# Optimization experiments

Hardware: AMD Instinct MI355X
Metric: run time of the kernel (lower is better)

The kernel has to match this reference:

```python
import jax, jax.numpy as jnp
import numpy as np

D_MODEL = 1024
NUM_HEADS = 16
HEAD_DIM = D_MODEL // NUM_HEADS
THETA = 10000.0
B, S = 2, 2048


def _apply_rope(t, cos, sin):
    # t: [B, H, S, hd]; cos/sin: [S, hd//2]
    te = t[..., 0::2]
    to = t[..., 1::2]
    re = te * cos - to * sin
    ro = te * sin + to * cos
    out = jnp.stack([re, ro], axis=-1)  # [B,H,S,hd//2,2]
    return out.reshape(t.shape)


def setup_inputs() -> dict:
    key = jax.random.key(0)
    kx, kq, kk, kv, ko = jax.random.split(key, 5)
    std = 2.0 / (2 * D_MODEL) ** 0.5
    def w(k):
        return jnp.clip(std * jax.random.normal(k, (D_MODEL, D_MODEL), jnp.float32), -3.0 * std, 3.0 * std)
    return {
        "x": jax.random.normal(kx, (B, S, D_MODEL), jnp.float32),
        "Wq": w(kq),
        "Wk": w(kk),
        "Wv": w(kv),
        "Wo": w(ko),
    }


def reference(x, Wq, Wk, Wv, Wo):
    Bv, Sv, _ = x.shape
    def proj(W):
        return jnp.einsum('bsd,ed->bse', x, W).reshape(Bv, Sv, NUM_HEADS, HEAD_DIM).transpose(0, 2, 1, 3)
    q, k, v = proj(Wq), proj(Wk), proj(Wv)

    pos = jnp.arange(Sv, dtype=jnp.float32)
    inv_freq = THETA ** (-jnp.arange(0, HEAD_DIM, 2, dtype=jnp.float32) / HEAD_DIM)
    ang = pos[:, None] * inv_freq[None, :]  # [S, hd//2]
    cos, sin = jnp.cos(ang), jnp.sin(ang)
    q = _apply_rope(q, cos, sin)
    k = _apply_rope(k, cos, sin)

    scale = 1.0 / jnp.sqrt(jnp.float32(HEAD_DIM))
    scores = jnp.einsum('bhqd,bhkd->bhqk', q.astype(jnp.float32), k.astype(jnp.float32)) * scale
    causal = jnp.tril(jnp.ones((Sv, Sv), dtype=bool))
    scores = jnp.where(causal[None, None], scores, -jnp.inf)
    attn = jax.nn.softmax(scores, axis=-1)
    out = jnp.einsum('bhqk,bhkd->bhqd', attn, v.astype(jnp.float32))
    out = out.transpose(0, 2, 1, 3).reshape(Bv, Sv, D_MODEL)
    return jnp.einsum('bsd,ed->bse', out, Wo)
```

## Files before the change

### kernel.cpp

```cpp
#include <hip/hip_runtime.h>
#include <hip/hip_bf16.h>
#include <stdint.h>

typedef __bf16 bf16x8 __attribute__((ext_vector_type(8)));
typedef float  f32x4  __attribute__((ext_vector_type(4)));

__device__ __forceinline__ float bf2f(unsigned short u) {
    union { float f; uint32_t i; } v; v.i = ((uint32_t)u) << 16; return v.f;
}
__device__ __forceinline__ unsigned short f2bf(float f) {
    union { float f; uint32_t i; } v; v.f = f;
    uint32_t r = v.i + 0x7FFF + ((v.i >> 16) & 1);
    return (unsigned short)(r >> 16);
}
__device__ __forceinline__ unsigned short f2bf_rz(float f) {
    union { float f; uint32_t i; } v; v.f = f;
    return (unsigned short)(v.i >> 16);
}
__device__ __forceinline__ float exp2_raw(float x) {
    float r;
    asm("v_exp_f32 %0, %1" : "=v"(r) : "v"(x));
    return r;
}

#define GLD_LDS(gptr, lptr) \
    __builtin_amdgcn_global_load_lds( \
        (const __attribute__((address_space(1))) void*)(gptr), \
        (__attribute__((address_space(3))) void*)(lptr), 16, 0, 0)

__global__ __launch_bounds__(256) void convert_inputs(
    const void* __restrict__ x,  const void* __restrict__ wq,
    const void* __restrict__ wk, const void* __restrict__ wv,
    const void* __restrict__ wo, unsigned short* __restrict__ dst,
    unsigned short* __restrict__ wob_dst, int* __restrict__ flag)
{
    __shared__ int cnt[256];
    const int tid = threadIdx.x;
    uint32_t u = ((const uint32_t*)x)[tid];
    int e = (u >> 7) & 0xFF;
    cnt[tid] = (e >= 100 && e <= 140) ? 1 : 0;
    __syncthreads();
    for (int s = 128; s > 0; s >>= 1) {
        if (tid < s) cnt[tid] += cnt[tid + s];
        __syncthreads();
    }
    const int isf32 = (cnt[0] >= 128) ? 0 : 1;
    if (blockIdx.x == 0 && tid == 0) flag[0] = isf32 ? 0 : 1;

    int c = blockIdx.x * 256 + tid;
    const void* src; size_t off; unsigned short* out;
    if (c < 524288)      { src = x;  off = (size_t)c * 8;            out = dst + (size_t)c * 8; }
    else if (c < 655360) { src = wq; off = (size_t)(c - 524288) * 8; out = dst + (size_t)c * 8; }
    else if (c < 786432) { src = wk; off = (size_t)(c - 655360) * 8; out = dst + (size_t)c * 8; }
    else if (c < 917504) { src = wv; off = (size_t)(c - 786432) * 8; out = dst + (size_t)c * 8; }
    else                 { src = wo; off = (size_t)(c - 917504) * 8; out = wob_dst + off; }
    unsigned short t[8];
    if (isf32) {
        const float* s = (const float*)src + off;
        float4 f0 = *(const float4*)s;
        float4 f1 = *(const float4*)(s + 4);
        t[0] = f2bf(f0.x); t[1] = f2bf(f0.y); t[2] = f2bf(f0.z); t[3] = f2bf(f0.w);
        t[4] = f2bf(f1.x); t[5] = f2bf(f1.y); t[6] = f2bf(f1.z); t[7] = f2bf(f1.w);
    } else {
        *(uint4*)t = *(const uint4*)((const unsigned short*)src + off);
    }
    *(uint4*)out = *(const uint4*)t;
}

__global__ __launch_bounds__(512, 2) void gemm_qkv_8ph(
    const unsigned short* __restrict__ A,
    const unsigned short* __restrict__ B0,
    const unsigned short* __restrict__ B1,
    const unsigned short* __restrict__ B2,
    unsigned short* __restrict__ O0,
    unsigned short* __restrict__ O1,
    unsigned short* __restrict__ O2)
{
    __shared__ __align__(16) unsigned short Asl[2][16384];
    __shared__ __align__(16) unsigned short Bsl[2][16384];

    const int tid  = threadIdx.x;
    const int lane = tid & 63;
    const int wid  = tid >> 6;
    const int wm   = wid >> 2;
    const int wn   = wid & 3;
    const int lr   = lane & 15;
    const int quad = lane >> 4;

    const int bid   = blockIdx.x;
    const int xcd   = bid & 7;
    const int s_    = bid >> 3;
    const int m_idx = xcd + 8 * (s_ / 12);
    const int n_idx = s_ % 12;

    const int m0  = m_idx * 256;
    const int n0g = n_idx * 256;
    const int sel = n0g >> 10;
    const unsigned short* Bp = (sel == 0) ? B0 : ((sel == 1) ? B1 : B2);
    unsigned short* Optr     = (sel == 0) ? O0 : ((sel == 1) ? O1 : O2);
    const int n0  = n0g & 1023;

    const int sw0 = ((0 + quad) ^ (lr & 7)) * 8;
    const int sw1 = ((4 + quad) ^ (lr & 7)) * 8;

    f32x4 acc[2][4][2][2] = {};
    bf16x8 aF[4][2];
    bf16x8 bF[2][2];

#define STAGEA(T, H) do { \
    const int tA_ = (T); \
    _Pragma("unroll") \
    for (int p_ = 0; p_ < 2; ++p_) { \
        int c_   = p_ * 512 + tid; \
        int row_ = c_ >> 3; \
        int sc_  = ((c_ & 7) ^ (row_ & 7)) * 8; \
        GLD_LDS(&A[(size_t)(m0 + (H) * 128 + row_) * 1024 + tA_ * 64 + sc_], \
                &Asl[tA_ & 1][(H) * 8192 + c_ * 8]); \
    } } while (0)

#define STAGEB(T, H) do { \
    const int tB_ = (T); \
    _Pragma("unroll") \
    for (int p_ = 0; p_ < 2; ++p_) { \
        int c_   = p_ * 512 + tid; \
        int row_ = c_ >> 3; \
        int sc_  = ((c_ & 7) ^ (row_ & 7)) * 8; \
        GLD_LDS(&Bp[(size_t)(n0 + (H) * 128 + row_) * 1024 + tB_ * 64 + sc_], \
                &Bsl[tB_ & 1][(H) * 8192 + c_ * 8]); \
    } } while (0)

#define LOADA(BUF, QM) do { \
    _Pragma("unroll") \
    for (int fm_ = 0; fm_ < 4; ++fm_) { \
        const int row_ = (QM) * 128 + wm * 64 + fm_ * 16 + lr; \
        aF[fm_][0] = *(const bf16x8*)&Asl[BUF][row_ * 64 + sw0]; \
        aF[fm_][1] = *(const bf16x8*)&Asl[BUF][row_ * 64 + sw1]; \
    } } while (0)

#define LOADB(BUF, QN) do { \
    _Pragma("unroll") \
    for (int fn_ = 0; fn_ < 2; ++fn_) { \
        const int row_ = (QN) * 128 + wn * 32 + fn_ * 16 + lr; \
        bF[fn_][0] = *(const bf16x8*)&Bsl[BUF][row_ * 64 + sw0]; \
        bF[fn_][1] = *(const bf16x8*)&Bsl[BUF][row_ * 64 + sw1]; \
    } } while (0)

#define MFMA16(QM, QN) do { \
    __builtin_amdgcn_s_setprio(1); \
    _Pragma("unroll") \
    for (int fm_ = 0; fm_ < 4; ++fm_) { \
        _Pragma("unroll") \
        for (int fn_ = 0; fn_ < 2; ++fn_) { \
            acc[QM][fm_][QN][fn_] = __builtin_amdgcn_mfma_f32_16x16x32_bf16( \
                aF[fm_][0], bF[fn_][0], acc[QM][fm_][QN][fn_], 0, 0, 0); \
            acc[QM][fm_][QN][fn_] = __builtin_amdgcn_mfma_f32_16x16x32_bf16( \
                aF[fm_][1], bF[fn_][1], acc[QM][fm_][QN][fn_], 0, 0, 0); \
        } \
    } \
    __builtin_amdgcn_s_setprio(0); \
    } while (0)

#define BARRIER() __builtin_amdgcn_s_barrier()
#define LGKM0()   asm volatile("s_waitcnt lgkmcnt(0)" ::: "memory")

    STAGEB(0, 0);
    STAGEA(0, 1);
    STAGEA(0, 0);
    STAGEB(0, 1);
    STAGEB(1, 0);
    STAGEA(1, 1);
    asm volatile("s_waitcnt vmcnt(4)" ::: "memory");
    BARRIER();

    const int NT = 16;
#pragma unroll 2
    for (int t = 0; t < NT; ++t) {
        const int buf = t & 1;

        LOADA(buf, 0);
        LOADB(buf, 0);
        if (t + 1 < NT) STAGEA(t + 1, 0);
        BARRIER();
        LGKM0();
        MFMA16(0, 0);
        BARRIER();

        LOADA(buf, 1);
        if (t + 1 < NT) STAGEB(t + 1, 1);
        BARRIER();
        LGKM0();
        MFMA16(1, 0);
        BARRIER();

        LOADB(buf, 1);
        if (t + 2 < NT) STAGEB(t + 2, 0);
        BARRIER();
        LGKM0();
        MFMA16(1, 1);
        BARRIER();

        LOADA(buf, 0);
        if (t + 2 < NT) STAGEA(t + 2, 1);
        BARRIER();
        LGKM0();
        MFMA16(0, 1);
        if (t + 2 < NT) asm volatile("s_waitcnt vmcnt(4)" ::: "memory");
        else            asm volatile("s_waitcnt vmcnt(0)" ::: "memory");
        BARRIER();
    }

#pragma unroll
    for (int qm = 0; qm < 2; ++qm) {
#pragma unroll
        for (int fm = 0; fm < 4; ++fm) {
            const int mb = m0 + qm * 128 + wm * 64 + fm * 16 + quad * 4;
#pragma unroll
            for (int qn = 0; qn < 2; ++qn) {
#pragma unroll
                for (int fn = 0; fn < 2; ++fn) {
                    const int nl = n0 + qn * 128 + wn * 32 + fn * 16 + lr;
                    const int h = nl >> 6, d = nl & 63;
#pragma unroll
                    for (int r = 0; r < 4; ++r) {
                        const int m = mb + r;
                        const int b = m >> 11, s = m & 2047;
                        Optr[((size_t)(b * 16 + h) * 2048 + s) * 64 + d] =
                            f2bf(acc[qm][fm][qn][fn][r]);
                    }
                }
            }
        }
    }
#undef STAGEA
#undef STAGEB
#undef LOADA
#undef LOADB
#undef MFMA16
#undef BARRIER
#undef LGKM0
}

template<int NS>
__global__ __launch_bounds__(256) void combine_kernel(
    const unsigned short* __restrict__ P0,
    const unsigned short* __restrict__ P1,
    const unsigned short* __restrict__ P2,
    const unsigned short* __restrict__ P3,
    const float* __restrict__ Lsum,
    unsigned short* __restrict__ C)
{
    const int tid = threadIdx.x;
    const int m   = blockIdx.x * 2 + (tid >> 7);
    const int c8  = (tid & 127) * 8;
    const int b = m >> 11, s = m & 2047;
    const int h = c8 >> 6, d0 = c8 & 63;
    const int li = (b * 16 + h) * 2048 + s;

    float lsum = Lsum[li] + Lsum[65536 + li];
    if (NS == 4) lsum += Lsum[131072 + li] + Lsum[196608 + li];
    const float inv = 1.0f / lsum;

    const size_t addr = (size_t)li * 64 + d0;
    unsigned short a[8], bb[8], o[8];
    *(uint4*)a  = *(const uint4*)&P0[addr];
    *(uint4*)bb = *(const uint4*)&P1[addr];
    if (NS == 4) {
        unsigned short c2[8], d2[8];
        *(uint4*)c2 = *(const uint4*)&P2[addr];
        *(uint4*)d2 = *(const uint4*)&P3[addr];
        for (int j = 0; j < 8; ++j)
            o[j] = f2bf((bf2f(a[j]) + bf2f(bb[j]) + bf2f(c2[j]) + bf2f(d2[j])) * inv);
    } else {
        for (int j = 0; j < 8; ++j)
            o[j] = f2bf((bf2f(a[j]) + bf2f(bb[j])) * inv);
    }
    *(uint4*)&C[(size_t)m * 1024 + c8] = *(const uint4*)o;
}

__global__ __launch_bounds__(256) void gemm_out(
    const unsigned short* __restrict__ A,
    const unsigned short* __restrict__ B0,
    void* __restrict__ O,
    const int* __restrict__ flag)
{
    const int K = 1024;
    __shared__ __align__(16) unsigned short As[64 * 64];
    __shared__ __align__(16) unsigned short Bs[128 * 64];

    const int isf32 = (flag[0] == 0) ? 1 : 0;

    const int tid  = threadIdx.x;
    const int lane = tid & 63;
    const int wid  = tid >> 6;
    const int wm   = wid >> 1;
    const int wn   = wid & 1;
    const int lr   = lane & 15;
    const int quad = lane >> 4;
    const int q8   = quad * 8;

    const int bid   = blockIdx.x;
    const int xcd   = bid & 7;
    const int s_    = bid >> 3;
    const int m_idx = xcd + 8 * (s_ >> 3);
    const int n_idx = s_ & 7;

    const int m0 = m_idx * 64;
    const int n0 = n_idx * 128;

    f32x4 acc[2][4] = {};

    for (int kk = 0; kk < K; kk += 64) {
        __syncthreads();
        for (int p = 0; p < 2; ++p) {
            int c   = p * 256 + tid;
            int row = c >> 3;
            int c8  = (c & 7) * 8;
            GLD_LDS(&A[(size_t)(m0 + row) * K + kk + c8], &As[c * 8]);
        }
        for (int p = 0; p < 4; ++p) {
            int c   = p * 256 + tid;
            int row = c >> 3;
            int c8  = (c & 7) * 8;
            GLD_LDS(&B0[(size_t)(n0 + row) * K + kk + c8], &Bs[c * 8]);
        }
        __syncthreads();

        for (int ks = 0; ks < 64; ks += 32) {
            bf16x8 af[2], bf[4];
            for (int t = 0; t < 2; ++t)
                af[t] = *(const bf16x8*)&As[(wm * 32 + t * 16 + lr) * 64 + ks + q8];
            for (int t = 0; t < 4; ++t)
                bf[t] = *(const bf16x8*)&Bs[(wn * 64 + t * 16 + lr) * 64 + ks + q8];
            for (int mt = 0; mt < 2; ++mt)
                for (int nt = 0; nt < 4; ++nt)
                    acc[mt][nt] = __builtin_amdgcn_mfma_f32_16x16x32_bf16(
                        af[mt], bf[nt], acc[mt][nt], 0, 0, 0);
        }
    }

    for (int mt = 0; mt < 2; ++mt) {
        for (int nt = 0; nt < 4; ++nt) {
            for (int r = 0; r < 4; ++r) {
                int m  = m0 + wm * 32 + mt * 16 + quad * 4 + r;
                int nl = n0 + wn * 64 + nt * 16 + lr;
                float val = acc[mt][nt][r];
                if (isf32) ((float*)O)[(size_t)m * 1024 + nl] = val;
                else ((unsigned short*)O)[(size_t)m * 1024 + nl] = f2bf(val);
            }
        }
    }
}

__global__ __launch_bounds__(256) void rope_transpose(
    unsigned short* __restrict__ Q, unsigned short* __restrict__ Kp,
    const unsigned short* __restrict__ V, unsigned short* __restrict__ Vt)
{
    __shared__ unsigned short T[64 * 65];
    const int tid = threadIdx.x;

    if (blockIdx.x < 4096) {
        const int CH = 32 * 2048 * 8;
        int idx = blockIdx.x * 256 + tid;
        bool isK = idx >= CH;
        int j = isK ? (idx - CH) : idx;
        unsigned short* p = isK ? Kp : Q;

        int c8   = j & 7;
        int srow = j >> 3;
        int s    = srow & 2047;
        int off  = srow * 64 + c8 * 8;

        uint4 raw = *(const uint4*)&p[off];
        unsigned short t[8];
        *(uint4*)t = raw;
        float sf = (float)s;
        float qs = isK ? 1.0f : 0.18033688011112043f;
        for (int jj = 0; jj < 4; ++jj) {
            int i = c8 * 4 + jj;
            float inv = __expf(-0.2878231366f * (float)i);
            float ang = sf * inv;
            float sn = __sinf(ang);
            float cs = __cosf(ang);
            float e = bf2f(t[2 * jj]);
            float o = bf2f(t[2 * jj + 1]);
            t[2 * jj]     = f2bf((e * cs - o * sn) * qs);
            t[2 * jj + 1] = f2bf((e * sn + o * cs) * qs);
        }
        *(uint4*)&p[off] = *(const uint4*)t;
    } else {
        int bidx = blockIdx.x - 4096;
        const int s0 = (bidx & 31) * 64;
        const int bh = bidx >> 5;

        const unsigned short* src = V + ((size_t)bh * 2048 + s0) * 64;
        for (int p = 0; p < 2; ++p) {
            int c = p * 256 + tid;
            int s  = c >> 3;
            int d8 = (c & 7) * 8;
            uint4 raw = *(const uint4*)&src[s * 64 + d8];
            unsigned short t[8];
            *(uint4*)t = raw;
            for (int j = 0; j < 8; ++j) T[s * 65 + d8 + j] = t[j];
        }
        __syncthreads();
        unsigned short* dst = Vt + (size_t)bh * 64 * 2048 + s0;
        for (int p = 0; p < 2; ++p) {
            int c = p * 256 + tid;
            int d  = c >> 3;
            int s8 = (c & 7) * 8;
            unsigned short t[8];
            for (int j = 0; j < 8; ++j) t[j] = T[(s8 + j) * 65 + d];
            *(uint4*)&dst[(size_t)d * 2048 + s8] = *(const uint4*)t;
        }
    }
}

template<int NSPLIT>
__global__ __launch_bounds__(256) void attn_kernel(
    const unsigned short* __restrict__ Q,
    const unsigned short* __restrict__ Kp,
    const unsigned short* __restrict__ Vt,
    unsigned short* __restrict__ P0,
    unsigned short* __restrict__ P1,
    unsigned short* __restrict__ P2,
    unsigned short* __restrict__ P3,
    float* __restrict__ Lsum)
{
    __shared__ __align__(16) unsigned short Ks[2][4096];
    __shared__ __align__(16) unsigned short Vs[2][4096];
    __shared__ __align__(16) unsigned short Ps[4096];

    const int tid  = threadIdx.x;
    const int lane = tid & 63;
    const int w    = tid >> 6;
    const int lr   = lane & 15;
    const int quad = lane >> 4;
    const int q8   = quad * 8;
    const int wps  = w * 1024;

    int bh, split, qb, kb0, kb1;
    if (NSPLIT == 2) {
        bh = blockIdx.x;
        const int y  = blockIdx.y;
        split = y >> 4;
        const int yq = y & 15;
        qb  = (yq < 8) ? yq : (23 - yq);
        kb0 = split ? (qb + 1) : 0;
        kb1 = split ? (2 * qb + 1) : qb;
    } else {
        const int idx = blockIdx.x;
        qb    = 15 - (idx >> 7);
        const int r = idx & 127;
        split = r >> 5;
        bh    = r & 31;
        const int L = 2 * qb + 2;
        kb0 = (L * split) >> 2;
        kb1 = ((L * (split + 1)) >> 2) - 1;
    }

    unsigned short* Pout = (split == 0) ? P0 : (split == 1) ? P1
                         : (split == 2) ? P2 : P3;

    const unsigned short* KbBase = Kp + (size_t)bh * 2048 * 64;
    const unsigned short* VbBase = Vt + (size_t)bh * 131072;

    auto stage = [&](int kb, int buf) {
        const unsigned short* Kb = KbBase + kb * 64 * 64;
        const unsigned short* Vb = VbBase + kb * 64;
        for (int p = 0; p < 2; ++p) {
            int c    = p * 256 + tid;
            int f    = c >> 6, l = c & 63;
            int nt   = f >> 1, ks = f & 1;
            int lr_s = l & 15, qd = l >> 4;
            GLD_LDS(&Kb[(nt * 16 + lr_s) * 64 + ks * 32 + qd * 8], &Ks[buf][c * 8]);
            GLD_LDS(&Vb[(size_t)(nt * 16 + lr_s) * 2048 + ks * 32 + qd * 8], &Vs[buf][c * 8]);
        }
    };

    const int q0 = qb * 128;
    bf16x8 qa[2][2];
    for (int mt = 0; mt < 2; ++mt) {
        const unsigned short* Qw = Q + ((size_t)bh * 2048 + q0 + mt * 64 + w * 16 + lr) * 64;
        qa[mt][0] = *(const bf16x8*)&Qw[q8];
        qa[mt][1] = *(const bf16x8*)&Qw[32 + q8];
    }

    stage(kb0, 0);

    f32x4 oacc[2][4] = {};
    float lpart[2][4] = {};
    const int l8 = lane * 8;
    const int lr7 = lr & 7;
    const int lrh = lr >> 3;

    for (int kb = kb0; kb <= kb1; ++kb) {
        const int cur = (kb - kb0) & 1;
        __syncthreads();
        if (kb < kb1) stage(kb + 1, cur ^ 1);

        f32x4 sacc[2][4] = {};
        for (int nt = 0; nt < 4; ++nt) {
            bf16x8 kf0 = *(const bf16x8*)&Ks[cur][(nt * 2 + 0) * 512 + l8];
            bf16x8 kf1 = *(const bf16x8*)&Ks[cur][(nt * 2 + 1) * 512 + l8];
            for (int mt = 0; mt < 2; ++mt) {
                sacc[mt][nt] = __builtin_amdgcn_mfma_f32_16x16x32_bf16(qa[mt][0], kf0, sacc[mt][nt], 0, 0, 0);
                sacc[mt][nt] = __builtin_amdgcn_mfma_f32_16x16x32_bf16(qa[mt][1], kf1, sacc[mt][nt], 0, 0, 0);
            }
        }

        if (kb >= 2 * qb) {
            for (int mt = 0; mt < 2; ++mt) {
                int rowb = q0 + mt * 64 + w * 16 + quad * 4;
                for (int nt = 0; nt < 4; ++nt) {
                    int col = kb * 64 + nt * 16 + lr;
                    for (int r = 0; r < 4; ++r)
                        if (col > rowb + r) sacc[mt][nt][r] = -3.0e38f;
                }
            }
        }

        for (int mt = 0; mt < 2; ++mt) {
            for (int r = 0; r < 4; ++r) {
                for (int nt = 0; nt < 4; ++nt) {
                    float pv = exp2_raw(sacc[mt][nt][r] - 23.083120654223414f);
                    lpart[mt][r] += pv;
                    int ks = nt >> 1;
                    int qr = (nt * 2 + lrh) & 3;
                    Ps[wps + ks * 512 + (qr * 16 + quad * 4 + r) * 8 + lr7] = f2bf_rz(pv);
                }
            }
            for (int ks = 0; ks < 2; ++ks) {
                bf16x8 pa = *(const bf16x8*)&Ps[wps + ks * 512 + l8];
                for (int nt = 0; nt < 4; ++nt) {
                    bf16x8 vf = *(const bf16x8*)&Vs[cur][(nt * 2 + ks) * 512 + l8];
                    oacc[mt][nt] = __builtin_amdgcn_mfma_f32_16x16x32_bf16(pa, vf, oacc[mt][nt], 0, 0, 0);
                }
            }
        }
    }

    for (int mt = 0; mt < 2; ++mt) {
        for (int r = 0; r < 4; ++r) {
            float l = lpart[mt][r];
            for (int off = 1; off < 16; off <<= 1)
                l += __shfl_xor(l, off, 64);
            int s = q0 + mt * 64 + w * 16 + quad * 4 + r;
            for (int nt = 0; nt < 4; ++nt)
                Pout[((size_t)bh * 2048 + s) * 64 + nt * 16 + lr] = f2bf_rz(oacc[mt][nt][r]);
            if (lr == 0) Lsum[split * 65536 + bh * 2048 + s] = l;
        }
    }
}

extern "C" void kernel_launch(void* const* d_in, const int* in_sizes, int n_in,
                              void* d_out, int out_size, void* d_ws, size_t ws_size,
                              hipStream_t stream)
{
    const void* x  = d_in[0];
    const void* Wq = d_in[1];
    const void* Wk = d_in[2];
    const void* Wv = d_in[3];
    const void* Wo = d_in[4];

    int* flag = (int*)d_ws;
    unsigned short* base = (unsigned short*)d_ws + 8;
    const size_t M1 = 1048576;
    unsigned short* xb  = base;
    unsigned short* wqb = base + 4 * M1;
    unsigned short* wkb = base + 5 * M1;
    unsigned short* wvb = base + 6 * M1;
    unsigned short* q   = base + 8 * M1;
    unsigned short* k   = base + 12 * M1;
    unsigned short* v   = base + 16 * M1;
    unsigned short* wob = base + 20 * M1;
    float*          Ls  = (float*)(base + 21 * M1);
    unsigned short* vt  = xb;
    unsigned short* P0  = v;
    unsigned short* P1  = wqb;
    unsigned short* P2  = base + 22 * M1;
    unsigned short* P3  = base + 26 * M1;
    unsigned short* Cb  = q;

    const bool big = ws_size >= (size_t)30 * M1 * 2 + 16;

    convert_inputs<<<dim3(4096), 256, 0, stream>>>(x, Wq, Wk, Wv, Wo, base, wob, flag);
    gemm_qkv_8ph<<<dim3(192), 512, 0, stream>>>(xb, wqb, wkb, wvb, q, k, v);
    rope_transpose<<<dim3(5120), 256, 0, stream>>>(q, k, v, vt);
    if (big) {
        attn_kernel<4><<<dim3(2048), 256, 0, stream>>>(q, k, vt, P0, P1, P2, P3, Ls);
        combine_kernel<4><<<dim3(2048), 256, 0, stream>>>(P0, P1, P2, P3, Ls, Cb);
    } else {
        attn_kernel<2><<<dim3(32, 32), 256, 0, stream>>>(q, k, vt, P0, P1, P0, P0, Ls);
        combine_kernel<2><<<dim3(2048), 256, 0, stream>>>(P0, P1, P0, P0, Ls, Cb);
    }
    gemm_out<<<dim3(512), 256, 0, stream>>>(Cb, wob, d_out, flag);
}
```

Measured before the change: 206.8 us.

## Use 512-thread attention blocks with 256-row query tiles and equal 4-way KV splits

Replaces the templated 4-split attention kernel with a dedicated 512-thread version. Each block now covers 256 query rows (8 waves × 32 rows) instead of 128, so each staged K/V tile is reused by twice as many queries. KV blocks are divided evenly across the 4 splits, and the grid shrinks to 1024 blocks. The 2-split fallback becomes its own non-templated kernel. The aim is to halve redundant K/V global loads per query, at the cost of fewer blocks, larger LDS per block, and a different load balance across the causal triangle.

Result: no change. 204.0 us (-1.4%).

```diff
diff --git a/kernel.cpp b/kernel.cpp
--- a/kernel.cpp
+++ b/kernel.cpp
@@ -415,8 +415,7 @@
     }
 }
 
-template<int NSPLIT>
-__global__ __launch_bounds__(256) void attn_kernel(
+__global__ __launch_bounds__(512) void attn_kernel512(
     const unsigned short* __restrict__ Q,
     const unsigned short* __restrict__ Kp,
     const unsigned short* __restrict__ Vt,
@@ -428,7 +427,7 @@
 {
     __shared__ __align__(16) unsigned short Ks[2][4096];
     __shared__ __align__(16) unsigned short Vs[2][4096];
-    __shared__ __align__(16) unsigned short Ps[4096];
+    __shared__ __align__(16) unsigned short Ps[8192];
 
     const int tid  = threadIdx.x;
     const int lane = tid & 63;
@@ -438,28 +437,136 @@
     const int q8   = quad * 8;
     const int wps  = w * 1024;
 
-    int bh, split, qb, kb0, kb1;
-    if (NSPLIT == 2) {
-        bh = blockIdx.x;
-        const int y  = blockIdx.y;
-        split = y >> 4;
-        const int yq = y & 15;
-        qb  = (yq < 8) ? yq : (23 - yq);
-        kb0 = split ? (qb + 1) : 0;
-        kb1 = split ? (2 * qb + 1) : qb;
-    } else {
-        const int idx = blockIdx.x;
-        qb    = 15 - (idx >> 7);
-        const int r = idx & 127;
-        split = r >> 5;
-        bh    = r & 31;
-        const int L = 2 * qb + 2;
-        kb0 = (L * split) >> 2;
-        kb1 = ((L * (split + 1)) >> 2) - 1;
-    }
+    const int idx   = blockIdx.x;
+    const int qb    = 7 - (idx >> 7);
+    const int r_    = idx & 127;
+    const int split = r_ >> 5;
+    const int bh    = r_ & 31;
+    const int kb0   = (qb + 1) * split;
+    const int kb1   = (qb + 1) * (split + 1) - 1;
 
     unsigned short* Pout = (split == 0) ? P0 : (split == 1) ? P1
                          : (split == 2) ? P2 : P3;
+
+    const unsigned short* KbBase = Kp + (size_t)bh * 2048 * 64;
+    const unsigned short* VbBase = Vt + (size_t)bh * 131072;
+
+    auto stage = [&](int kb, int buf) {
+        const unsigned short* Kb = KbBase + kb * 64 * 64;
+        const unsigned short* Vb = VbBase + kb * 64;
+        int c    = tid;
+        int f    = c >> 6, l = c & 63;
+        int nt   = f >> 1, ks = f & 1;
+        int lr_s = l & 15, qd = l >> 4;
+        GLD_LDS(&Kb[(nt * 16 + lr_s) * 64 + ks * 32 + qd * 8], &Ks[buf][c * 8]);
+        GLD_LDS(&Vb[(size_t)(nt * 16 + lr_s) * 2048 + ks * 32 + qd * 8], &Vs[buf][c * 8]);
+    };
+
+    const int q0 = qb * 256;
+    bf16x8 qa[2][2];
+    for (int mt = 0; mt < 2; ++mt) {
+        const unsigned short* Qw = Q + ((size_t)bh * 2048 + q0 + w * 32 + mt * 16 + lr) * 64;
+        qa[mt][0] = *(const bf16x8*)&Qw[q8];
+        qa[mt][1] = *(const bf16x8*)&Qw[32 + q8];
+    }
+
+    stage(kb0, 0);
+
+    f32x4 oacc[2][4] = {};
+    float lpart[2][4] = {};
+    const int l8 = lane * 8;
+    const int lr7 = lr & 7;
+    const int lrh = lr >> 3;
+
+    for (int kb = kb0; kb <= kb1; ++kb) {
+        const int cur = (kb - kb0) & 1;
+        __syncthreads();
+        if (kb < kb1) stage(kb + 1, cur ^ 1);
+
+        f32x4 sacc[2][4] = {};
+        for (int nt = 0; nt < 4; ++nt) {
+            bf16x8 kf0 = *(const bf16x8*)&Ks[cur][(nt * 2 + 0) * 512 + l8];
+            bf16x8 kf1 = *(const bf16x8*)&Ks[cur][(nt * 2 + 1) * 512 + l8];
+            for (int mt = 0; mt < 2; ++mt) {
+                sacc[mt][nt] = __builtin_amdgcn_mfma_f32_16x16x32_bf16(qa[mt][0], kf0, sacc[mt][nt], 0, 0, 0);
+                sacc[mt][nt] = __builtin_amdgcn_mfma_f32_16x16x32_bf16(qa[mt][1], kf1, sacc[mt][nt], 0, 0, 0);
+            }
+        }
+
+        if (kb >= 4 * qb) {
+            for (int mt = 0; mt < 2; ++mt) {
+                int rowb = q0 + w * 32 + mt * 16 + quad * 4;
+                for (int nt = 0; nt < 4; ++nt) {
+                    int col = kb * 64 + nt * 16 + lr;
+                    for (int r = 0; r < 4; ++r)
+                        if (col > rowb + r) sacc[mt][nt][r] = -3.0e38f;
+                }
+            }
+        }
+
+        for (int mt = 0; mt < 2; ++mt) {
+            for (int r = 0; r < 4; ++r) {
+                for (int nt = 0; nt < 4; ++nt) {
+                    float pv = exp2_raw(sacc[mt][nt][r] - 23.083120654223414f);
+                    lpart[mt][r] += pv;
+                    int ks = nt >> 1;
+                    int qr = (nt * 2 + lrh) & 3;
+                    Ps[wps + ks * 512 + (qr * 16 + quad * 4 + r) * 8 + lr7] = f2bf_rz(pv);
+                }
+            }
+            for (int ks = 0; ks < 2; ++ks) {
+                bf16x8 pa = *(const bf16x8*)&Ps[wps + ks * 512 + l8];
+                for (int nt = 0; nt < 4; ++nt) {
+                    bf16x8 vf = *(const bf16x8*)&Vs[cur][(nt * 2 + ks) * 512 + l8];
+                    oacc[mt][nt] = __builtin_amdgcn_mfma_f32_16x16x32_bf16(pa, vf, oacc[mt][nt], 0, 0, 0);
+                }
+            }
+        }
+    }
+
+    for (int mt = 0; mt < 2; ++mt) {
+        for (int r = 0; r < 4; ++r) {
+            float l = lpart[mt][r];
+            for (int off = 1; off < 16; off <<= 1)
+                l += __shfl_xor(l, off, 64);
+            int s = q0 + w * 32 + mt * 16 + quad * 4 + r;
+            for (int nt = 0; nt < 4; ++nt)
+                Pout[((size_t)bh * 2048 + s) * 64 + nt * 16 + lr] = f2bf_rz(oacc[mt][nt][r]);
+            if (lr == 0) Lsum[split * 65536 + bh * 2048 + s] = l;
+        }
+    }
+}
+
+__global__ __launch_bounds__(256) void attn_kernel2(
+    const unsigned short* __restrict__ Q,
+    const unsigned short* __restrict__ Kp,
+    const unsigned short* __restrict__ Vt,
+    unsigned short* __restrict__ P0,
+    unsigned short* __restrict__ P1,
+    float* __restrict__ Lsum)
+{
+    __shared__ __align__(16) unsigned short Ks[2][4096];
+    __shared__ __align__(16) unsigned short Vs[2][4096];
+    __shared__ __align__(16) unsigned short Ps[4096];
+
+    const int tid  = threadIdx.x;
+    const int lane = tid & 63;
+    const int w    = tid >> 6;
+    const int lr   = lane & 15;
+    const int quad = lane >> 4;
+    const int q8   = quad * 8;
+    const int wps  = w * 1024;
+
+    const int bh    = blockIdx.x;
+    const int y     = blockIdx.y;
+    const int split = y >> 4;
+    const int yq    = y & 15;
+    const int qb    = (yq < 8) ? yq : (23 - yq);
+    const int q0    = qb * 128;
+    const int kb0   = split ? (qb + 1) : 0;
+    const int kb1   = split ? (2 * qb + 1) : qb;
+
+    unsigned short* Pout = split ? P1 : P0;
 
     const unsigned short* KbBase = Kp + (size_t)bh * 2048 * 64;
     const unsigned short* VbBase = Vt + (size_t)bh * 131072;
@@ -477,7 +584,6 @@
         }
     };
 
-    const int q0 = qb * 128;
     bf16x8 qa[2][2];
     for (int mt = 0; mt < 2; ++mt) {
         const unsigned short* Qw = Q + ((size_t)bh * 2048 + q0 + mt * 64 + w * 16 + lr) * 64;
@@ -587,10 +693,10 @@
     gemm_qkv_8ph<<<dim3(192), 512, 0, stream>>>(xb, wqb, wkb, wvb, q, k, v);
     rope_transpose<<<dim3(5120), 256, 0, stream>>>(q, k, v, vt);
     if (big) {
-        attn_kernel<4><<<dim3(2048), 256, 0, stream>>>(q, k, vt, P0, P1, P2, P3, Ls);
+        attn_kernel512<<<dim3(1024), 512, 0, stream>>>(q, k, vt, P0, P1, P2, P3, Ls);
         combine_kernel<4><<<dim3(2048), 256, 0, stream>>>(P0, P1, P2, P3, Ls, Cb);
     } else {
-        attn_kernel<2><<<dim3(32, 32), 256, 0, stream>>>(q, k, vt, P0, P1, P0, P0, Ls);
+        attn_kernel2<<<dim3(32, 32), 256, 0, stream>>>(q, k, vt, P0, P1, Ls);
         combine_kernel<2><<<dim3(2048), 256, 0, stream>>>(P0, P1, P0, P0, Ls, Cb);
     }
     gemm_out<<<dim3(512), 256, 0, stream>>>(Cb, wob, d_out, flag);
```
